# Kernel tuning notes

Measured on AMD Instinct MI355X. Metric: run time of the kernel, lower is better.

Reference implementation:

```python
import jax, jax.numpy as jnp
import numpy as np

ALPHA = (0.02, 0.04, 0.08, 0.16)
CHAMFER_W, SMOOTH_W, CURVATURE_W = 1.0, 1.0, 0.3
NS = (8192, 4096, 2048, 1024)
B = 2


def _sqdist(a, b):
    # a: [B,N,3], b: [B,M,3] -> [B,N,M] squared euclidean distance
    return (jnp.sum(a * a, axis=-1)[:, :, None]
            - 2.0 * jnp.einsum('bnc,bmc->bnm', a, b)
            + jnp.sum(b * b, axis=-1)[:, None, :])


def _knn(d, k):
    # k smallest distances + indices along last axis
    neg, idx = jax.lax.top_k(-d, k)
    return -neg, idx


def _gather(points, idx):
    # points: [B,M,C], idx: [B,N,K] -> [B,N,K,C]
    return jax.vmap(lambda p, i: p[i])(points, idx)


def _scale_loss(pc1, pc2, flow):
    # pc1, pc2, flow: [B,3,N]-like -> permute to points-last layout
    p1 = jnp.transpose(pc1, (0, 2, 1))   # [B,N,3]
    p2 = jnp.transpose(pc2, (0, 2, 1))   # [B,M,3]
    fl = jnp.transpose(flow, (0, 2, 1))  # [B,N,3]
    warp = p1 + fl                        # warped pc1

    # curvature of pc2 (10-NN on pc2 itself)
    _, k22 = _knn(_sqdist(p2, p2), 10)
    cv2 = jnp.sum(_gather(p2, k22) - p2[:, :, None, :], axis=2) / 9.0  # [B,M,3]

    # 10-NN on pc1 (shared for warped curvature and smoothness; 9-NN is prefix)
    _, k11 = _knn(_sqdist(p1, p1), 10)
    cvw = jnp.sum(_gather(warp, k11) - warp[:, :, None, :], axis=2) / 9.0  # [B,N,3]

    k9 = k11[:, :, :9]
    gfl = _gather(fl, k9)  # [B,N,9,3]
    smooth = jnp.sum(jnp.linalg.norm(gfl - fl[:, :, None, :], axis=3), axis=2) / 8.0  # [B,N]

    # chamfer between warped pc1 and pc2
    d12 = _sqdist(warp, p2)               # [B,N,M]
    dist1 = jnp.min(d12, axis=-1)         # [B,N]
    dist2 = jnp.min(d12, axis=1)          # [B,M]

    # inverse-distance interpolation of pc2 curvature onto warped pc1 (5-NN)
    dist, kidx = _knn(d12, 5)             # [B,N,5]
    gcv = _gather(cv2, kidx)              # [B,N,5,3]
    w = 1.0 / (dist + 1e-8)
    w = w / jnp.sum(w, axis=2, keepdims=True)
    inter = jnp.sum(w[..., None] * gcv, axis=2)  # [B,N,3]

    chamfer = jnp.mean(jnp.sum(dist1, axis=1)) + jnp.mean(jnp.sum(dist2, axis=1))
    smoothness = jnp.mean(jnp.sum(smooth, axis=1))
    curv = jnp.mean(jnp.sum(jnp.sum((inter - cvw) ** 2, axis=2), axis=1))
    return chamfer, smoothness, curv


def setup_inputs() -> dict:
    key = jax.random.key(0)
    keys = jax.random.split(key, 12)
    out = {}
    names = ['pc1', 'pc2', 'flow']
    k = 0
    for name in names:
        for i, n in enumerate(NS):
            scale = 1.0 if name != 'flow' else 0.1
            out[f'{name}_{i}'] = scale * jax.random.normal(keys[k], (B, 3, n), dtype=jnp.float32)
            k += 1
    return out


def reference(pc1_0, pc1_1, pc1_2, pc1_3,
              pc2_0, pc2_1, pc2_2, pc2_3,
              flow_0, flow_1, flow_2, flow_3):
    pcs1 = (pc1_0, pc1_1, pc1_2, pc1_3)
    pcs2 = (pc2_0, pc2_1, pc2_2, pc2_3)
    flows = (flow_0, flow_1, flow_2, flow_3)
    ch = sm = cv = jnp.float32(0.0)
    for a, p1, p2, fl in zip(ALPHA, pcs1, pcs2, flows):
        c, s, k = _scale_loss(p1, p2, fl)
        ch = ch + a * c
        sm = sm + a * s
        cv = cv + a * k
    total = CHAMFER_W * ch + CURVATURE_W * cv + SMOOTH_W * sm
    return jnp.reshape(total, (1,))
```

## Files before the change

### kernel.cpp

```cpp
#include <hip/hip_runtime.h>
#include <math.h>


#define UNIT 1024
#define NTOT 15360
#define MASKC 0xFFFFE000u
#define NTASK 2380u

typedef unsigned int uint;
typedef __attribute__((ext_vector_type(8))) float f8;

struct Params {
  const float* pc1[4];
  const float* pc2[4];
  const float* fl[4];
  float4* cv2;
  float4* cvw;
  float* keys;
  uint* d2u;
  uint* cnt;
  float* out;
};


__device__ __forceinline__ float wave_sum(float v) {
  #pragma unroll
  for (int o = 32; o; o >>= 1) v += __shfl_down(v, o, 64);
  return v;
}

template <int K>
__device__ __forceinline__ void key_insert(float (&kd)[K], float kf) {
  #pragma unroll
  for (int m = K - 1; m >= 1; --m)
    kd[m] = __builtin_amdgcn_fmed3f(kf, kd[m - 1], kd[m]);
  kd[0] = fminf(kd[0], kf);
}

template <int K>
__device__ __forceinline__ void merge_pair(float (&a)[K], const float (&b)[K]) {
  #pragma unroll
  for (int m = 0; m < K; ++m) key_insert<K>(a, b[m]);
}

__device__ __forceinline__ float pack_key_u(float d, uint iw) {
  return __uint_as_float((__float_as_uint(d) & MASKC) | iw);
}

__device__ __forceinline__ void sload3(const float* px, const float* py,
                                       const float* pz, int boff,
                                       f8& x, f8& y, f8& z) {
  asm volatile(
      "s_load_dwordx8 %0, %3, %6\n\t"
      "s_load_dwordx8 %1, %4, %6\n\t"
      "s_load_dwordx8 %2, %5, %6\n\t"
      "s_waitcnt lgkmcnt(0)"
      : "=&s"(x), "=&s"(y), "=&s"(z)
      : "s"(px), "s"(py), "s"(pz), "s"(boff));
}

__device__ __forceinline__ void sload6(const float* px, const float* py,
                                       const float* pz, const float* fx,
                                       const float* fy, const float* fz,
                                       int boff, f8& x, f8& y, f8& z,
                                       f8& u, f8& v, f8& w) {
  asm volatile(
      "s_load_dwordx8 %0, %6, %12\n\t"
      "s_load_dwordx8 %1, %7, %12\n\t"
      "s_load_dwordx8 %2, %8, %12\n\t"
      "s_load_dwordx8 %3, %9, %12\n\t"
      "s_load_dwordx8 %4, %10, %12\n\t"
      "s_load_dwordx8 %5, %11, %12\n\t"
      "s_waitcnt lgkmcnt(0)"
      : "=&s"(x), "=&s"(y), "=&s"(z), "=&s"(u), "=&s"(v), "=&s"(w)
      : "s"(px), "s"(py), "s"(pz), "s"(fx), "s"(fy), "s"(fz), "s"(boff));
}

template <int K>
__device__ void scan_k(const float* px, const float* py, const float* pz,
                       int lo, float ax, float ay, float az,
                       float (&a)[K], float (&b)[K]) {
  #pragma unroll 1
  for (int c0 = 0; c0 < UNIT; c0 += 8) {
    f8 xs, ys, zs;
    sload3(px, py, pz, (lo + c0) * 4, xs, ys, zs);
    #pragma unroll
    for (int t = 0; t < 8; t += 2) {
      float dxa = xs[t] - ax, dya = ys[t] - ay, dza = zs[t] - az;
      float dA = fmaf(dxa, dxa, fmaf(dya, dya, dza * dza));
      float dxb = xs[t + 1] - ax, dyb = ys[t + 1] - ay, dzb = zs[t + 1] - az;
      float dB = fmaf(dxb, dxb, fmaf(dyb, dyb, dzb * dzb));
      key_insert<K>(a, pack_key_u(dA, (uint)(lo + c0 + t)));
      key_insert<K>(b, pack_key_u(dB, (uint)(lo + c0 + t + 1)));
    }
  }
}

__device__ void scan_w256(const float* px, const float* py, const float* pz,
                          const float* fx, const float* fy, const float* fz,
                          int lo, float ax, float ay, float az,
                          float& a0, float& b0) {
  #pragma unroll 1
  for (int c0 = 0; c0 < 256; c0 += 8) {
    f8 xs, ys, zs, us, vs, ws;
    sload6(px, py, pz, fx, fy, fz, (lo + c0) * 4, xs, ys, zs, us, vs, ws);
    #pragma unroll
    for (int t = 0; t < 8; t += 2) {
      float cxa = xs[t] + us[t], cya = ys[t] + vs[t], cza = zs[t] + ws[t];
      float dxa = cxa - ax, dya = cya - ay, dza = cza - az;
      float dA = fmaf(dxa, dxa, fmaf(dya, dya, dza * dza));
      float cxb = xs[t + 1] + us[t + 1], cyb = ys[t + 1] + vs[t + 1],
            czb = zs[t + 1] + ws[t + 1];
      float dxb = cxb - ax, dyb = cyb - ay, dzb = czb - az;
      float dB = fmaf(dxb, dxb, fmaf(dyb, dyb, dzb * dzb));
      a0 = fminf(a0, dA);
      b0 = fminf(b0, dB);
    }
  }
}

__device__ __forceinline__ void decode(int r, int wv, int& s, int& b,
                                       int& i0, int& lo, int& N, int& cpw,
                                       int& off, float& alpha) {
  int rr;
  if (r < 256)      { s = 0; rr = r; }
  else if (r < 320) { s = 1; rr = r - 256; }
  else if (r < 336) { s = 2; rr = r - 320; }
  else              { s = 3; rr = r - 336; }
  N = 8192 >> s;
  cpw = 8 >> s;
  int perb = 128 >> (2 * s);
  b = rr >> (7 - 2 * s);
  int chunk = rr & (perb - 1);
  int qg = (chunk << s) + (wv >> (3 - s));
  i0 = qg << 6;
  lo = (wv & (cpw - 1)) << 10;
  off = 16384 - (16384 >> s);
  alpha = 0.02f * (float)(1 << s);
}

template <int K>
__device__ __forceinline__ bool merge_group(float (&a)[K], float* sm,
                                            int tid, int cpw) {
  const int STR = K | 1;
  int q = tid & 63, wv = tid >> 6;
  #pragma unroll
  for (int m = 0; m < K; ++m) sm[(wv * 64 + q) * STR + m] = a[m];
  __syncthreads();
  if (wv & (cpw - 1)) return false;
  for (int w = wv + 1; w < wv + cpw; ++w)
    #pragma unroll
    for (int m = 0; m < K; ++m)
      key_insert<K>(a, sm[(w * 64 + q) * STR + m]);
  return true;
}


__global__ __launch_bounds__(256) void k_init(Params P) {
  int t = blockIdx.x * 256 + threadIdx.x;
  if (t == 0) { P.out[0] = 0.f; *P.cnt = 1024u; }
  if (t < 2 * NTOT) P.d2u[t] = 0x7F7FFFFFu;
}

__global__ __launch_bounds__(512, 8) void k_work(Params P) {
  __shared__ float sm[8 * 64 * 11];
  __shared__ uint ts;
  int tid = threadIdx.x, q = tid & 63, wv = tid >> 6;

  uint t = blockIdx.x;
  while (t < NTASK) {
    if (t < 1020u) {
      int pass = (int)t / 340, r = (int)t % 340;
      int s, b, i0, lo, N, cpw, off; float alpha;
      decode(r, wv, s, b, i0, lo, N, cpw, off, alpha);
      int i = i0 + q;
      int lo_u = __builtin_amdgcn_readfirstlane(lo);

      if (pass == 0) {
        const float* p2 = P.pc2[s] + b * 3 * N;
        float ax = p2[i], ay = p2[N + i], az = p2[2 * N + i];
        float a[10], bb[10];
        #pragma unroll
        for (int m = 0; m < 10; ++m) { a[m] = 3.0e38f; bb[m] = 3.0e38f; }
        scan_k<10>(p2, p2 + N, p2 + 2 * N, lo_u, ax, ay, az, a, bb);
        merge_pair<10>(a, bb);
        if (merge_group<10>(a, sm, tid, cpw)) {
          float sx = 0.f, sy = 0.f, sz = 0.f;
          #pragma unroll
          for (int m = 0; m < 10; ++m) {
            int j = (int)(__float_as_uint(a[m]) & 0x1FFFu);
            sx += p2[j]; sy += p2[N + j]; sz += p2[2 * N + j];
          }
          const float inv9 = 1.f / 9.f;
          P.cv2[b * NTOT + off + i] = make_float4((sx - 10.f * ax) * inv9,
                                                  (sy - 10.f * ay) * inv9,
                                                  (sz - 10.f * az) * inv9,
                                                  0.f);
        }
      } else if (pass == 1) {
        const float* p1 = P.pc1[s] + b * 3 * N;
        const float* fl = P.fl[s] + b * 3 * N;
        float ax = p1[i], ay = p1[N + i], az = p1[2 * N + i];
        float a[10], bb[10];
        #pragma unroll
        for (int m = 0; m < 10; ++m) { a[m] = 3.0e38f; bb[m] = 3.0e38f; }
        scan_k<10>(p1, p1 + N, p1 + 2 * N, lo_u, ax, ay, az, a, bb);
        merge_pair<10>(a, bb);
        if (merge_group<10>(a, sm, tid, cpw)) {
          float fix = fl[i], fiy = fl[N + i], fiz = fl[2 * N + i];
          float wix = ax + fix, wiy = ay + fiy, wiz = az + fiz;
          float sx = 0.f, sy = 0.f, sz = 0.f, smooth = 0.f;
          float dmax = -1.f, worst = 0.f;
          #pragma unroll
          for (int m = 0; m < 10; ++m) {
            int j = (int)(__float_as_uint(a[m]) & 0x1FFFu);
            float px = p1[j], py = p1[N + j], pz = p1[2 * N + j];
            float flx = fl[j], fly = fl[N + j], flz = fl[2 * N + j];
            sx += px + flx; sy += py + fly; sz += pz + flz;
            float ddx = px - ax, ddy = py - ay, ddz = pz - az;
            float d = fmaf(ddx, ddx, fmaf(ddy, ddy, ddz * ddz));
            float gx = flx - fix, gy = fly - fiy, gz = flz - fiz;
            float term = sqrtf(fmaf(gx, gx, fmaf(gy, gy, gz * gz)));
            smooth += term;
            if (d > dmax) { dmax = d; worst = term; }
          }
          smooth -= worst;
          const float inv9 = 1.f / 9.f;
          P.cvw[b * NTOT + off + i] = make_float4((sx - 10.f * wix) * inv9,
                                                  (sy - 10.f * wiy) * inv9,
                                                  (sz - 10.f * wiz) * inv9,
                                                  0.f);
          float ssum = wave_sum(smooth * (1.f / 8.f));
          if (q == 0) atomicAdd(P.out, alpha * 0.5f * ssum);
        }
      } else {
        const float* p1 = P.pc1[s] + b * 3 * N;
        const float* fl = P.fl[s] + b * 3 * N;
        const float* p2 = P.pc2[s] + b * 3 * N;
        float ax = p1[i] + fl[i], ay = p1[N + i] + fl[N + i],
              az = p1[2 * N + i] + fl[2 * N + i];
        float a[5], bb[5];
        #pragma unroll
        for (int m = 0; m < 5; ++m) { a[m] = 3.0e38f; bb[m] = 3.0e38f; }
        scan_k<5>(p2, p2 + N, p2 + 2 * N, lo_u, ax, ay, az, a, bb);
        merge_pair<5>(a, bb);
        if (merge_group<5>(a, sm, tid, cpw)) {
          #pragma unroll
          for (int m = 0; m < 5; ++m)
            P.keys[m * (2 * NTOT) + b * NTOT + off + i] = a[m];
        }
      }
    } else {
      int dm = (int)(t - 1020u);
      int s, tb;
      if (dm < 1024)      { s = 0; tb = dm; }
      else if (dm < 1280) { s = 1; tb = dm - 1024; }
      else if (dm < 1344) { s = 2; tb = dm - 1280; }
      else                { s = 3; tb = dm - 1344; }
      int N = 8192 >> s;
      int tpb = 512 >> (2 * s);
      int b = tb >> (9 - 2 * s);
      int ti = tb & (tpb - 1);
      int u = ti * 8 + wv;
      int rpq = 32 >> s;
      int qg = u >> (5 - s);
      int rg = u & (rpq - 1);
      int i = qg * 64 + q, lo = rg * 256;
      int off = 16384 - (16384 >> s);
      const float* p1 = P.pc1[s] + b * 3 * N;
      const float* fl = P.fl[s] + b * 3 * N;
      const float* p2 = P.pc2[s] + b * 3 * N;
      float ax = p2[i], ay = p2[N + i], az = p2[2 * N + i];
      float a0 = 3.0e38f, b0 = 3.0e38f;
      int lo_u = __builtin_amdgcn_readfirstlane(lo);
      scan_w256(p1, p1 + N, p1 + 2 * N, fl, fl + N, fl + 2 * N,
                lo_u, ax, ay, az, a0, b0);
      atomicMin(P.d2u + b * NTOT + off + i, __float_as_uint(fminf(a0, b0)));
    }
    __syncthreads();
    if (tid == 0) ts = atomicAdd(P.cnt, 1u);
    __syncthreads();
    t = ts;
  }
}

__global__ __launch_bounds__(256) void k_epi(Params P) {
  int t = blockIdx.x * 256 + threadIdx.x;
  int b = t >= NTOT;
  int r = t - b * NTOT;
  int s, i;
  if (r < 8192)       { s = 0; i = r; }
  else if (r < 12288) { s = 1; i = r - 8192; }
  else if (r < 14336) { s = 2; i = r - 12288; }
  else                { s = 3; i = r - 14336; }
  int N = 8192 >> s;
  int off = 16384 - (16384 >> s);
  float alpha = 0.02f * (float)(1 << s);
  const float* p1 = P.pc1[s] + b * 3 * N;
  const float* fl = P.fl[s] + b * 3 * N;
  const float* p2 = P.pc2[s] + b * 3 * N;
  float ax = p1[i] + fl[i], ay = p1[N + i] + fl[N + i],
        az = p1[2 * N + i] + fl[2 * N + i];
  float dist1 = 3.0e38f, wsum = 0.f, ix = 0.f, iy = 0.f, iz = 0.f;
  #pragma unroll
  for (int m = 0; m < 5; ++m) {
    uint key = __float_as_uint(P.keys[m * (2 * NTOT) + b * NTOT + off + i]);
    int j = (int)(key & 0x1FFFu);
    float px = p2[j], py = p2[N + j], pz = p2[2 * N + j];
    float ddx = px - ax, ddy = py - ay, ddz = pz - az;
    float d = fmaf(ddx, ddx, fmaf(ddy, ddy, ddz * ddz));
    dist1 = fminf(dist1, d);
    float w = 1.f / (d + 1e-8f);
    wsum += w;
    float4 cv = P.cv2[b * NTOT + off + j];
    ix += w * cv.x; iy += w * cv.y; iz += w * cv.z;
  }
  float inv = 1.f / wsum;
  ix *= inv; iy *= inv; iz *= inv;
  float4 cw = P.cvw[b * NTOT + off + i];
  float ex = ix - cw.x, ey = iy - cw.y, ez = iz - cw.z;
  float curv = fmaf(ex, ex, fmaf(ey, ey, ez * ez));
  float csum = wave_sum(dist1 + 0.3f * curv);
  float msum = wave_sum(__uint_as_float(P.d2u[t]));
  if ((threadIdx.x & 63) == 0) {
    atomicAdd(P.out, alpha * 0.5f * csum);
    atomicAdd(P.out, alpha * 0.5f * msum);
  }
}

extern "C" void kernel_launch(void* const* d_in, const int* in_sizes, int n_in,
                              void* d_out, int out_size, void* d_ws,
                              size_t ws_size, hipStream_t stream) {
  Params P;
  for (int s = 0; s < 4; ++s) {
    P.pc1[s] = (const float*)d_in[s];
    P.pc2[s] = (const float*)d_in[4 + s];
    P.fl[s]  = (const float*)d_in[8 + s];
  }
  char* ws = (char*)d_ws;
  P.cv2  = (float4*)ws;
  P.cvw  = (float4*)(ws + 491520);
  P.keys = (float*)(ws + 983040);
  P.d2u  = (uint*)(ws + 1597440);
  P.cnt  = (uint*)(ws + 1720320);
  P.out  = (float*)d_out;

  k_init<<<dim3(120), dim3(256), 0, stream>>>(P);
  k_work<<<dim3(1024), dim3(512), 0, stream>>>(P);
  k_epi<<<dim3(120), dim3(256), 0, stream>>>(P);
}
```

Measured before the change: 312.5 us.

## Precompute warped pc1 in init kernel and widen scalar loads to dwordx16

The init kernel now computes warp = pc1 + flow into a workspace buffer. The chamfer and pc2-to-warp scans then read that buffer instead of loading both pc1 and flow and adding them per element. The scalar load helpers are widened from dwordx8 to dwordx16, so each iteration processes 16 candidates and has half as many loop iterations and waits. The cost is a larger init grid plus an extra global write and read of the warp buffer, and higher SGPR pressure from the wider loads.

```diff
diff --git a/kernel.cpp b/kernel.cpp
--- a/kernel.cpp
+++ b/kernel.cpp
@@ -8,7 +8,7 @@
 #define NTASK 2380u
 
 typedef unsigned int uint;
-typedef __attribute__((ext_vector_type(8))) float f8;
+typedef __attribute__((ext_vector_type(16))) float f16v;
 
 struct Params {
   const float* pc1[4];
@@ -19,6 +19,7 @@
   float* keys;
   uint* d2u;
   uint* cnt;
+  float* warp;
   float* out;
 };
 
@@ -47,33 +48,16 @@
   return __uint_as_float((__float_as_uint(d) & MASKC) | iw);
 }
 
-__device__ __forceinline__ void sload3(const float* px, const float* py,
-                                       const float* pz, int boff,
-                                       f8& x, f8& y, f8& z) {
+__device__ __forceinline__ void sload3x16(const float* px, const float* py,
+                                          const float* pz, int boff,
+                                          f16v& x, f16v& y, f16v& z) {
   asm volatile(
-      "s_load_dwordx8 %0, %3, %6\n\t"
-      "s_load_dwordx8 %1, %4, %6\n\t"
-      "s_load_dwordx8 %2, %5, %6\n\t"
+      "s_load_dwordx16 %0, %3, %6\n\t"
+      "s_load_dwordx16 %1, %4, %6\n\t"
+      "s_load_dwordx16 %2, %5, %6\n\t"
       "s_waitcnt lgkmcnt(0)"
       : "=&s"(x), "=&s"(y), "=&s"(z)
       : "s"(px), "s"(py), "s"(pz), "s"(boff));
-}
-
-__device__ __forceinline__ void sload6(const float* px, const float* py,
-                                       const float* pz, const float* fx,
-                                       const float* fy, const float* fz,
-                                       int boff, f8& x, f8& y, f8& z,
-                                       f8& u, f8& v, f8& w) {
-  asm volatile(
-      "s_load_dwordx8 %0, %6, %12\n\t"
-      "s_load_dwordx8 %1, %7, %12\n\t"
-      "s_load_dwordx8 %2, %8, %12\n\t"
-      "s_load_dwordx8 %3, %9, %12\n\t"
-      "s_load_dwordx8 %4, %10, %12\n\t"
-      "s_load_dwordx8 %5, %11, %12\n\t"
-      "s_waitcnt lgkmcnt(0)"
-      : "=&s"(x), "=&s"(y), "=&s"(z), "=&s"(u), "=&s"(v), "=&s"(w)
-      : "s"(px), "s"(py), "s"(pz), "s"(fx), "s"(fy), "s"(fz), "s"(boff));
 }
 
 template <int K>
@@ -81,11 +65,11 @@
                        int lo, float ax, float ay, float az,
                        float (&a)[K], float (&b)[K]) {
   #pragma unroll 1
-  for (int c0 = 0; c0 < UNIT; c0 += 8) {
-    f8 xs, ys, zs;
-    sload3(px, py, pz, (lo + c0) * 4, xs, ys, zs);
+  for (int c0 = 0; c0 < UNIT; c0 += 16) {
+    f16v xs, ys, zs;
+    sload3x16(px, py, pz, (lo + c0) * 4, xs, ys, zs);
     #pragma unroll
-    for (int t = 0; t < 8; t += 2) {
+    for (int t = 0; t < 16; t += 2) {
       float dxa = xs[t] - ax, dya = ys[t] - ay, dza = zs[t] - az;
       float dA = fmaf(dxa, dxa, fmaf(dya, dya, dza * dza));
       float dxb = xs[t + 1] - ax, dyb = ys[t + 1] - ay, dzb = zs[t + 1] - az;
@@ -96,22 +80,18 @@
   }
 }
 
-__device__ void scan_w256(const float* px, const float* py, const float* pz,
-                          const float* fx, const float* fy, const float* fz,
-                          int lo, float ax, float ay, float az,
-                          float& a0, float& b0) {
+__device__ void scan_m(const float* px, const float* py, const float* pz,
+                       int lo, int len, float ax, float ay, float az,
+                       float& a0, float& b0) {
   #pragma unroll 1
-  for (int c0 = 0; c0 < 256; c0 += 8) {
-    f8 xs, ys, zs, us, vs, ws;
-    sload6(px, py, pz, fx, fy, fz, (lo + c0) * 4, xs, ys, zs, us, vs, ws);
+  for (int c0 = 0; c0 < len; c0 += 16) {
+    f16v xs, ys, zs;
+    sload3x16(px, py, pz, (lo + c0) * 4, xs, ys, zs);
     #pragma unroll
-    for (int t = 0; t < 8; t += 2) {
-      float cxa = xs[t] + us[t], cya = ys[t] + vs[t], cza = zs[t] + ws[t];
-      float dxa = cxa - ax, dya = cya - ay, dza = cza - az;
+    for (int t = 0; t < 16; t += 2) {
+      float dxa = xs[t] - ax, dya = ys[t] - ay, dza = zs[t] - az;
       float dA = fmaf(dxa, dxa, fmaf(dya, dya, dza * dza));
-      float cxb = xs[t + 1] + us[t + 1], cyb = ys[t + 1] + vs[t + 1],
-            czb = zs[t + 1] + ws[t + 1];
-      float dxb = cxb - ax, dyb = cyb - ay, dzb = czb - az;
+      float dxb = xs[t + 1] - ax, dyb = ys[t + 1] - ay, dzb = zs[t + 1] - az;
       float dB = fmaf(dxb, dxb, fmaf(dyb, dyb, dzb * dzb));
       a0 = fminf(a0, dA);
       b0 = fminf(b0, dB);
@@ -160,6 +140,14 @@
   int t = blockIdx.x * 256 + threadIdx.x;
   if (t == 0) { P.out[0] = 0.f; *P.cnt = 1024u; }
   if (t < 2 * NTOT) P.d2u[t] = 0x7F7FFFFFu;
+  int s, r;
+  if (t < 49152)      { s = 0; r = t; }
+  else if (t < 73728) { s = 1; r = t - 49152; }
+  else if (t < 86016) { s = 2; r = t - 73728; }
+  else if (t < 92160) { s = 3; r = t - 86016; }
+  else return;
+  int base6 = (s == 0) ? 0 : (s == 1) ? 49152 : (s == 2) ? 73728 : 86016;
+  P.warp[base6 + r] = P.pc1[s][r] + P.fl[s][r];
 }
 
 __global__ __launch_bounds__(512, 8) void k_work(Params P) {
@@ -234,11 +222,11 @@
           if (q == 0) atomicAdd(P.out, alpha * 0.5f * ssum);
         }
       } else {
-        const float* p1 = P.pc1[s] + b * 3 * N;
-        const float* fl = P.fl[s] + b * 3 * N;
+        int base6 = (s == 0) ? 0 : (s == 1) ? 49152 : (s == 2) ? 73728
+                                                               : 86016;
+        const float* wq = P.warp + base6 + b * 3 * N;
         const float* p2 = P.pc2[s] + b * 3 * N;
-        float ax = p1[i] + fl[i], ay = p1[N + i] + fl[N + i],
-              az = p1[2 * N + i] + fl[2 * N + i];
+        float ax = wq[i], ay = wq[N + i], az = wq[2 * N + i];
         float a[5], bb[5];
         #pragma unroll
         for (int m = 0; m < 5; ++m) { a[m] = 3.0e38f; bb[m] = 3.0e38f; }
@@ -267,14 +255,14 @@
       int rg = u & (rpq - 1);
       int i = qg * 64 + q, lo = rg * 256;
       int off = 16384 - (16384 >> s);
-      const float* p1 = P.pc1[s] + b * 3 * N;
-      const float* fl = P.fl[s] + b * 3 * N;
+      int base6 = (s == 0) ? 0 : (s == 1) ? 49152 : (s == 2) ? 73728
+                                                             : 86016;
+      const float* wc = P.warp + base6 + b * 3 * N;
       const float* p2 = P.pc2[s] + b * 3 * N;
       float ax = p2[i], ay = p2[N + i], az = p2[2 * N + i];
       float a0 = 3.0e38f, b0 = 3.0e38f;
       int lo_u = __builtin_amdgcn_readfirstlane(lo);
-      scan_w256(p1, p1 + N, p1 + 2 * N, fl, fl + N, fl + 2 * N,
-                lo_u, ax, ay, az, a0, b0);
+      scan_m(wc, wc + N, wc + 2 * N, lo_u, 256, ax, ay, az, a0, b0);
       atomicMin(P.d2u + b * NTOT + off + i, __float_as_uint(fminf(a0, b0)));
     }
     __syncthreads();
@@ -343,9 +331,10 @@
   P.keys = (float*)(ws + 983040);
   P.d2u  = (uint*)(ws + 1597440);
   P.cnt  = (uint*)(ws + 1720320);
+  P.warp = (float*)(ws + 1720384);
   P.out  = (float*)d_out;
 
-  k_init<<<dim3(120), dim3(256), 0, stream>>>(P);
+  k_init<<<dim3(360), dim3(256), 0, stream>>>(P);
   k_work<<<dim3(1024), dim3(512), 0, stream>>>(P);
   k_epi<<<dim3(120), dim3(256), 0, stream>>>(P);
 }
```

Measured after the change: 301.9 us. 3.4% less time.

## Restructure reverse-chamfer min tasks to reduce in shared memory, drop atomicMin buffer

Applied to the files above, without the earlier changes.

Reverse chamfer tasks are regrouped so each block covers one 64-query group, with its 8 waves splitting the full pc1 range. Partial minima are merged in shared memory and summed straight into the output, replacing per-element global atomicMin and the d2u buffer. The init kernel shrinks to a single-thread zero kernel, the kNN scan loads 16 points per scalar load, and the epilogue does one atomic per block. This cuts the task count and global atomics, but uses longer per-task scans and more scalar registers.

```diff
diff --git a/kernel.cpp b/kernel.cpp
--- a/kernel.cpp
+++ b/kernel.cpp
@@ -5,10 +5,12 @@
 #define UNIT 1024
 #define NTOT 15360
 #define MASKC 0xFFFFE000u
-#define NTASK 2380u
+#define NTASK 1500u
+#define NBLK 1024u
 
 typedef unsigned int uint;
 typedef __attribute__((ext_vector_type(8))) float f8;
+typedef __attribute__((ext_vector_type(16))) float f16v;
 
 struct Params {
   const float* pc1[4];
@@ -17,7 +19,6 @@
   float4* cv2;
   float4* cvw;
   float* keys;
-  uint* d2u;
   uint* cnt;
   float* out;
 };
@@ -47,13 +48,13 @@
   return __uint_as_float((__float_as_uint(d) & MASKC) | iw);
 }
 
-__device__ __forceinline__ void sload3(const float* px, const float* py,
-                                       const float* pz, int boff,
-                                       f8& x, f8& y, f8& z) {
+__device__ __forceinline__ void sload3x16(const float* px, const float* py,
+                                          const float* pz, int boff,
+                                          f16v& x, f16v& y, f16v& z) {
   asm volatile(
-      "s_load_dwordx8 %0, %3, %6\n\t"
-      "s_load_dwordx8 %1, %4, %6\n\t"
-      "s_load_dwordx8 %2, %5, %6\n\t"
+      "s_load_dwordx16 %0, %3, %6\n\t"
+      "s_load_dwordx16 %1, %4, %6\n\t"
+      "s_load_dwordx16 %2, %5, %6\n\t"
       "s_waitcnt lgkmcnt(0)"
       : "=&s"(x), "=&s"(y), "=&s"(z)
       : "s"(px), "s"(py), "s"(pz), "s"(boff));
@@ -81,11 +82,11 @@
                        int lo, float ax, float ay, float az,
                        float (&a)[K], float (&b)[K]) {
   #pragma unroll 1
-  for (int c0 = 0; c0 < UNIT; c0 += 8) {
-    f8 xs, ys, zs;
-    sload3(px, py, pz, (lo + c0) * 4, xs, ys, zs);
+  for (int c0 = 0; c0 < UNIT; c0 += 16) {
+    f16v xs, ys, zs;
+    sload3x16(px, py, pz, (lo + c0) * 4, xs, ys, zs);
     #pragma unroll
-    for (int t = 0; t < 8; t += 2) {
+    for (int t = 0; t < 16; t += 2) {
       float dxa = xs[t] - ax, dya = ys[t] - ay, dza = zs[t] - az;
       float dA = fmaf(dxa, dxa, fmaf(dya, dya, dza * dza));
       float dxb = xs[t + 1] - ax, dyb = ys[t + 1] - ay, dzb = zs[t + 1] - az;
@@ -96,12 +97,12 @@
   }
 }
 
-__device__ void scan_w256(const float* px, const float* py, const float* pz,
-                          const float* fx, const float* fy, const float* fz,
-                          int lo, float ax, float ay, float az,
-                          float& a0, float& b0) {
+__device__ void scan_w(const float* px, const float* py, const float* pz,
+                       const float* fx, const float* fy, const float* fz,
+                       int lo, int len, float ax, float ay, float az,
+                       float& a0, float& b0) {
   #pragma unroll 1
-  for (int c0 = 0; c0 < 256; c0 += 8) {
+  for (int c0 = 0; c0 < len; c0 += 8) {
     f8 xs, ys, zs, us, vs, ws;
     sload6(px, py, pz, fx, fy, fz, (lo + c0) * 4, xs, ys, zs, us, vs, ws);
     #pragma unroll
@@ -156,10 +157,9 @@
 }
 
 
-__global__ __launch_bounds__(256) void k_init(Params P) {
-  int t = blockIdx.x * 256 + threadIdx.x;
-  if (t == 0) { P.out[0] = 0.f; *P.cnt = 1024u; }
-  if (t < 2 * NTOT) P.d2u[t] = 0x7F7FFFFFu;
+__global__ __launch_bounds__(1) void k_zero(Params P) {
+  P.out[0] = 0.f;
+  P.cnt[0] = 0u;
 }
 
 __global__ __launch_bounds__(512, 8) void k_work(Params P) {
@@ -251,40 +251,44 @@
         }
       }
     } else {
-      int dm = (int)(t - 1020u);
+      int dt = (int)(t - 1020u);
       int s, tb;
-      if (dm < 1024)      { s = 0; tb = dm; }
-      else if (dm < 1280) { s = 1; tb = dm - 1024; }
-      else if (dm < 1344) { s = 2; tb = dm - 1280; }
-      else                { s = 3; tb = dm - 1344; }
+      if (dt < 256)      { s = 0; tb = dt; }
+      else if (dt < 384) { s = 1; tb = dt - 256; }
+      else if (dt < 448) { s = 2; tb = dt - 384; }
+      else               { s = 3; tb = dt - 448; }
       int N = 8192 >> s;
-      int tpb = 512 >> (2 * s);
-      int b = tb >> (9 - 2 * s);
-      int ti = tb & (tpb - 1);
-      int u = ti * 8 + wv;
-      int rpq = 32 >> s;
-      int qg = u >> (5 - s);
-      int rg = u & (rpq - 1);
-      int i = qg * 64 + q, lo = rg * 256;
-      int off = 16384 - (16384 >> s);
+      int qpb = N >> 6;
+      int b = tb >= qpb;
+      int qg = tb - b * qpb;
+      int i = qg * 64 + q;
+      int len = N >> 3;
+      int lo = wv * len;
+      float alpha = 0.02f * (float)(1 << s);
       const float* p1 = P.pc1[s] + b * 3 * N;
       const float* fl = P.fl[s] + b * 3 * N;
       const float* p2 = P.pc2[s] + b * 3 * N;
       float ax = p2[i], ay = p2[N + i], az = p2[2 * N + i];
       float a0 = 3.0e38f, b0 = 3.0e38f;
       int lo_u = __builtin_amdgcn_readfirstlane(lo);
-      scan_w256(p1, p1 + N, p1 + 2 * N, fl, fl + N, fl + 2 * N,
-                lo_u, ax, ay, az, a0, b0);
-      atomicMin(P.d2u + b * NTOT + off + i, __float_as_uint(fminf(a0, b0)));
+      scan_w(p1, p1 + N, p1 + 2 * N, fl, fl + N, fl + 2 * N,
+             lo_u, len, ax, ay, az, a0, b0);
+      float a[1];
+      a[0] = fminf(a0, b0);
+      if (merge_group<1>(a, sm, tid, 8)) {
+        float msum = wave_sum(a[0]);
+        if (q == 0) atomicAdd(P.out, alpha * 0.5f * msum);
+      }
     }
     __syncthreads();
-    if (tid == 0) ts = atomicAdd(P.cnt, 1u);
+    if (tid == 0) ts = NBLK + atomicAdd(P.cnt, 1u);
     __syncthreads();
     t = ts;
   }
 }
 
 __global__ __launch_bounds__(256) void k_epi(Params P) {
+  __shared__ float part[4];
   int t = blockIdx.x * 256 + threadIdx.x;
   int b = t >= NTOT;
   int r = t - b * NTOT;
@@ -320,11 +324,15 @@
   float4 cw = P.cvw[b * NTOT + off + i];
   float ex = ix - cw.x, ey = iy - cw.y, ez = iz - cw.z;
   float curv = fmaf(ex, ex, fmaf(ey, ey, ez * ez));
-  float csum = wave_sum(dist1 + 0.3f * curv);
-  float msum = wave_sum(__uint_as_float(P.d2u[t]));
-  if ((threadIdx.x & 63) == 0) {
-    atomicAdd(P.out, alpha * 0.5f * csum);
-    atomicAdd(P.out, alpha * 0.5f * msum);
+  float csum = wave_sum(alpha * 0.5f * (dist1 + 0.3f * curv));
+  int wv = threadIdx.x >> 6;
+  if ((threadIdx.x & 63) == 0) part[wv] = csum;
+  __syncthreads();
+  if (threadIdx.x == 0) {
+    float v = 0.f;
+    #pragma unroll
+    for (int m = 0; m < 4; ++m) v += part[m];
+    atomicAdd(P.out, v);
   }
 }
 
@@ -341,11 +349,10 @@
   P.cv2  = (float4*)ws;
   P.cvw  = (float4*)(ws + 491520);
   P.keys = (float*)(ws + 983040);
-  P.d2u  = (uint*)(ws + 1597440);
-  P.cnt  = (uint*)(ws + 1720320);
+  P.cnt  = (uint*)(ws + 1597440);
   P.out  = (float*)d_out;
 
-  k_init<<<dim3(120), dim3(256), 0, stream>>>(P);
-  k_work<<<dim3(1024), dim3(512), 0, stream>>>(P);
+  k_zero<<<dim3(1), dim3(1), 0, stream>>>(P);
+  k_work<<<dim3(NBLK), dim3(512), 0, stream>>>(P);
   k_epi<<<dim3(120), dim3(256), 0, stream>>>(P);
 }
```

After: 303.8 us. -2.8%, faster.
